# Performance work log

Measured on AMD Instinct MI355X. Metric: run time of the kernel, lower is better.

The kernel has to match this reference:

```python
import jax, jax.numpy as jnp
import numpy as np

B, T, F = 4096, 60, 64
H = 128          # num_hidden[0] == num_hidden[1]
FC1_IN, FC1_OUT = T * H, 512   # 7680 -> 512
LEN_OUT = 60


def setup_inputs() -> dict:
    key = jax.random.key(0)
    ks = jax.random.split(key, 14)
    s1 = 1.0 / np.sqrt(H)
    def u(k, shape, s):
        return jax.random.uniform(k, shape, jnp.float32, -s, s)
    return {
        "X_cont": jax.random.normal(ks[0], (B, T, F), jnp.float32),
        # LSTM layer 1 (PyTorch gate order i,f,g,o)
        "W_ih1": u(ks[1], (4 * H, F), s1),
        "W_hh1": u(ks[2], (4 * H, H), s1),
        "b_ih1": u(ks[3], (4 * H,), s1),
        "b_hh1": u(ks[4], (4 * H,), s1),
        # LSTM layer 2
        "W_ih2": u(ks[5], (4 * H, H), s1),
        "W_hh2": u(ks[6], (4 * H, H), s1),
        "b_ih2": u(ks[7], (4 * H,), s1),
        "b_hh2": u(ks[8], (4 * H,), s1),
        # FC head
        "W_fc1": u(ks[9], (FC1_OUT, FC1_IN), 1.0 / np.sqrt(FC1_IN)),
        "b_fc1": u(ks[10], (FC1_OUT,), 1.0 / np.sqrt(FC1_IN)),
        "W_fc2": u(ks[11], (LEN_OUT, FC1_OUT), 1.0 / np.sqrt(FC1_OUT)),
        "b_fc2": u(ks[12], (LEN_OUT,), 1.0 / np.sqrt(FC1_OUT)),
    }


def _lstm_layer(x, W_ih, W_hh, b_ih, b_hh):
    # x: [B,T,Fin]; zero initial (h,c); returns full hidden sequence [B,T,H]
    b, h = x.shape[0], W_hh.shape[1]
    # precompute input contribution for all timesteps (one big GEMM)
    xg = jnp.einsum('btf,gf->btg', x, W_ih) + b_ih + b_hh  # [B,T,4H]

    def step(carry, xt):
        hp, cp = carry
        g = xt + hp @ W_hh.T                                # [B,4H]
        i, f, gg, o = jnp.split(g, 4, axis=-1)
        i = jax.nn.sigmoid(i)
        f = jax.nn.sigmoid(f)
        gg = jnp.tanh(gg)
        o = jax.nn.sigmoid(o)
        c = f * cp + i * gg
        hn = o * jnp.tanh(c)
        return (hn, c), hn

    h0 = jnp.zeros((b, h), x.dtype)
    _, hs = jax.lax.scan(step, (h0, h0), jnp.swapaxes(xg, 0, 1))  # [T,B,H]
    return jnp.swapaxes(hs, 0, 1)


def reference(X_cont, W_ih1, W_hh1, b_ih1, b_hh1,
              W_ih2, W_hh2, b_ih2, b_hh2,
              W_fc1, b_fc1, W_fc2, b_fc2):
    b = X_cont.shape[0]
    h1 = _lstm_layer(X_cont, W_ih1, W_hh1, b_ih1, b_hh1)   # [B,T,H]
    h2 = _lstm_layer(h1, W_ih2, W_hh2, b_ih2, b_hh2)       # [B,T,H]
    flat = h2.reshape(b, -1)                               # [B, T*H] = [B,7680]
    fc1 = flat @ W_fc1.T + b_fc1                           # [B,512]
    fc2 = fc1 @ W_fc2.T + b_fc2                            # [B,length_out]
    return fc2.reshape(b, LEN_OUT, 1)
```

## Files before the change

### kernel.cpp

```cpp
#include <hip/hip_runtime.h>
#include <hip/hip_fp16.h>
#include <cstdint>

typedef _Float16 h16;
typedef _Float16 half8 __attribute__((ext_vector_type(8)));
typedef float floatx4 __attribute__((ext_vector_type(4)));

#define T_SZ 60
#define H_SZ 128
#define NB_FC1 7680

#define LOG2E  1.44269504088896340736f
#define LOG2E2 2.88539008177792681472f

__device__ __forceinline__ float sigm(float x) {
    float e = __builtin_amdgcn_exp2f(x * -LOG2E);
    return __builtin_amdgcn_rcpf(1.0f + e);
}
__device__ __forceinline__ float tanh_fast(float x) {
    float e = __builtin_amdgcn_exp2f(x * LOG2E2);
    return 1.0f - 2.0f * __builtin_amdgcn_rcpf(e + 1.0f);
}

template<int INDIM, bool IN_F32, bool FUSE_FC>
__global__ __launch_bounds__(512, 1)
void lstm_layer(const void* __restrict__ in_v,
                const float* __restrict__ W_ih,
                const float* __restrict__ W_hh,
                const float* __restrict__ b_ih,
                const float* __restrict__ b_hh,
                h16* __restrict__ h_out,
                const h16* __restrict__ Wc,
                const float* __restrict__ bcv,
                float* __restrict__ out)
{
    constexpr int KT_IN = INDIM / 32;
    __shared__ __align__(16) h16 hist[16][16][H_SZ];

    const int tid  = threadIdx.x;
    const int w    = tid >> 6;
    const int lane = tid & 63;
    const int lrow = lane & 15;
    const int lgrp = lane >> 4;
    const size_t base_row = (size_t)blockIdx.x * 16;

    half8 wf_in[4][KT_IN];
    half8 wf_hh[4][4];
    float bias[4];

    #pragma unroll
    for (int q = 0; q < 4; ++q) {
        const int n = (w + 8 * q) * 16 + lrow;
        bias[q] = b_ih[n] + b_hh[n];
        #pragma unroll
        for (int kt = 0; kt < KT_IN; ++kt) {
            const float* p = W_ih + (size_t)n * INDIM + kt * 32 + lgrp * 8;
            half8 v;
            #pragma unroll
            for (int j = 0; j < 8; ++j) v[j] = (h16)p[j];
            wf_in[q][kt] = v;
        }
        #pragma unroll
        for (int kt = 0; kt < 4; ++kt) {
            const float* p = W_hh + (size_t)n * H_SZ + kt * 32 + lgrp * 8;
            half8 v;
            #pragma unroll
            for (int j = 0; j < 8; ++j) v[j] = (h16)p[j];
            wf_hh[q][kt] = v;
        }
    }

    const float* inF = (const float*)in_v;
    const h16*   inH = (const h16*)in_v;

    floatx4 raw[KT_IN][2];
    half8   xs[KT_IN];

    auto load_x = [&](int t) {
        #pragma unroll
        for (int kt = 0; kt < KT_IN; ++kt) {
            if constexpr (IN_F32) {
                const float* p = inF + ((base_row + lrow) * T_SZ + t) * INDIM + kt * 32 + lgrp * 8;
                raw[kt][0] = *(const floatx4*)(p);
                raw[kt][1] = *(const floatx4*)(p + 4);
            } else {
                xs[kt] = *(const half8*)(inH + ((base_row + lrow) * T_SZ + t) * INDIM + kt * 32 + lgrp * 8);
            }
        }
    };

    auto get_x = [&](half8 (&xf)[KT_IN]) {
        #pragma unroll
        for (int kt = 0; kt < KT_IN; ++kt) {
            if constexpr (IN_F32) {
                const auto p0 = __builtin_amdgcn_cvt_pkrtz(raw[kt][0][0], raw[kt][0][1]);
                const auto p1 = __builtin_amdgcn_cvt_pkrtz(raw[kt][0][2], raw[kt][0][3]);
                const auto p2 = __builtin_amdgcn_cvt_pkrtz(raw[kt][1][0], raw[kt][1][1]);
                const auto p3 = __builtin_amdgcn_cvt_pkrtz(raw[kt][1][2], raw[kt][1][3]);
                half8 v;
                v[0] = (h16)p0[0]; v[1] = (h16)p0[1]; v[2] = (h16)p1[0]; v[3] = (h16)p1[1];
                v[4] = (h16)p2[0]; v[5] = (h16)p2[1]; v[6] = (h16)p3[0]; v[7] = (h16)p3[1];
                xf[kt] = v;
            } else {
                xf[kt] = xs[kt];
            }
        }
    };

    floatx4 c4 = {0.f, 0.f, 0.f, 0.f};
    const int colW = 16 * w + lrow;

    auto flush = [&](int t) {
        half8 vals[4];
        int   time[4], row[4], cg[4];
        #pragma unroll
        for (int s = 0; s < 4; ++s) {
            const int u = tid + 512 * s;
            time[s] = t - 7 + (u >> 8);
            row[s]  = (u >> 4) & 15;
            cg[s]   = u & 15;
            vals[s] = *(const half8*)&hist[time[s] & 15][row[s]][(cg[s] * 8) ^ ((row[s] & 7) << 3)];
        }
        #pragma unroll
        for (int s = 0; s < 4; ++s)
            *(half8*)(h_out + ((base_row + row[s]) * T_SZ + time[s]) * H_SZ + cg[s] * 8) = vals[s];
    };

    floatx4 accA[4], accB[4];
    load_x(0);
    {
        half8 xf[KT_IN];
        get_x(xf);
        #pragma unroll
        for (int q = 0; q < 4; ++q) accA[q] = floatx4{bias[q], bias[q], bias[q], bias[q]};
        #pragma unroll
        for (int kt = 0; kt < KT_IN; ++kt)
            #pragma unroll
            for (int q = 0; q < 4; ++q)
                accA[q] = __builtin_amdgcn_mfma_f32_16x16x32_f16(xf[kt], wf_in[q][kt], accA[q], 0, 0, 0);
        load_x(1);
    }

    auto step = [&](int t, floatx4 (&accC)[4], floatx4 (&accN)[4]) {
        half8 hf[4];
        const bool have_h = (t > 0);
        if (have_h) {
            const h16* hb = &hist[(t - 1) & 15][0][0];
            #pragma unroll
            for (int kt = 0; kt < 4; ++kt) {
                const int col0 = kt * 32 + lgrp * 8;
                hf[kt] = *(const half8*)(hb + lrow * H_SZ + (col0 ^ ((lrow & 7) << 3)));
            }
        }

        if (t + 1 < T_SZ) {
            half8 xf[KT_IN];
            get_x(xf);
            #pragma unroll
            for (int q = 0; q < 4; ++q) accN[q] = floatx4{bias[q], bias[q], bias[q], bias[q]};
            #pragma unroll
            for (int kt = 0; kt < KT_IN; ++kt)
                #pragma unroll
                for (int q = 0; q < 4; ++q)
                    accN[q] = __builtin_amdgcn_mfma_f32_16x16x32_f16(xf[kt], wf_in[q][kt], accN[q], 0, 0, 0);
            if (t + 2 < T_SZ) load_x(t + 2);
        }

        if (have_h) {
            #pragma unroll
            for (int kt = 0; kt < 4; ++kt)
                #pragma unroll
                for (int q = 0; q < 4; ++q)
                    accC[q] = __builtin_amdgcn_mfma_f32_16x16x32_f16(hf[kt], wf_hh[q][kt], accC[q], 0, 0, 0);
        }

        h16 hcast[4];
        #pragma unroll
        for (int r = 0; r < 4; ++r) {
            const float gi = sigm(accC[0][r]);
            const float gf = sigm(accC[1][r]);
            const float gg = tanh_fast(accC[2][r]);
            const float go = sigm(accC[3][r]);
            const float cc = gf * c4[r] + gi * gg;
            c4[r] = cc;
            hcast[r] = (h16)(go * tanh_fast(cc));
        }
        h16* hb2 = &hist[t & 15][0][0];
        #pragma unroll
        for (int r = 0; r < 4; ++r) {
            const int rowW = lgrp * 4 + r;
            hb2[rowW * H_SZ + (colW ^ ((rowW & 7) << 3))] = hcast[r];
        }

        asm volatile("s_waitcnt lgkmcnt(0)" ::: "memory");
        __builtin_amdgcn_s_barrier();
        asm volatile("" ::: "memory");

        if (((t & 7) == 7) || (t == T_SZ - 1)) flush(t);
    };

    #pragma unroll 1
    for (int tt = 0; tt < T_SZ; tt += 2) {
        step(tt,     accA, accB);
        step(tt + 1, accB, accA);
    }

    if constexpr (FUSE_FC) {
        __syncthreads();

        floatx4 afc[4];
        #pragma unroll
        for (int q = 0; q < 4; ++q) afc[q] = floatx4{0.f, 0.f, 0.f, 0.f};

        const h16* arow = h_out + (base_row + lrow) * NB_FC1;

        auto ld = [&](int i, half8& a, half8 (&b)[4]) {
            const int k0 = (w * 30 + i) * 32 + lgrp * 8;
            a = *(const half8*)(arow + k0);
            #pragma unroll
            for (int q = 0; q < 4; ++q) {
                const int n = q * 16 + lrow;
                b[q] = 0;
                if (n < 60) b[q] = *(const half8*)(Wc + (size_t)n * NB_FC1 + k0);
            }
        };
        auto mm4 = [&](const half8& a, const half8 (&b)[4]) {
            #pragma unroll
            for (int q = 0; q < 4; ++q)
                afc[q] = __builtin_amdgcn_mfma_f32_16x16x32_f16(a, b[q], afc[q], 0, 0, 0);
        };

        half8 a0, a1, a2, b0[4], b1[4], b2[4];
        ld(0, a0, b0);
        ld(1, a1, b1);
        #pragma unroll 1
        for (int i = 0; i < 30; i += 3) {
            ld(i + 2, a2, b2);
            mm4(a0, b0);
            if (i + 3 < 30) ld(i + 3, a0, b0);
            mm4(a1, b1);
            if (i + 4 < 30) ld(i + 4, a1, b1);
            mm4(a2, b2);
        }

        float* red = (float*)&hist[0][0][0];
        #pragma unroll
        for (int q = 0; q < 4; ++q)
            #pragma unroll
            for (int r = 0; r < 4; ++r)
                red[(((w * 4 + q) * 16) + (lgrp * 4 + r)) * 16 + lrow] = afc[q][r];
        __syncthreads();

        #pragma unroll
        for (int s = 0; s < 2; ++s) {
            const int idx = tid + 512 * s;
            const int row = idx >> 6, col = idx & 63;
            if (col < 60) {
                const int q = col >> 4, cin = col & 15;
                float v = 0.f;
                #pragma unroll
                for (int ww = 0; ww < 8; ++ww)
                    v += red[(((ww * 4 + q) * 16) + row) * 16 + cin];
                out[(base_row + row) * 60 + col] = v + bcv[col];
            }
        }
    }
}

__global__ __launch_bounds__(256, 2)
void head_kernel(const float* __restrict__ W_fc1,
                 const float* __restrict__ W_fc2,
                 const float* __restrict__ b_fc1,
                 const float* __restrict__ b_fc2,
                 h16* __restrict__ Wc,
                 float* __restrict__ bc)
{
    const int tid  = threadIdx.x;
    if (blockIdx.x >= 120) {
        const int m = blockIdx.x - 120;
        const int t = tid;
        float p = W_fc2[m * 512 + t] * b_fc1[t] + W_fc2[m * 512 + 256 + t] * b_fc1[256 + t];
        #pragma unroll
        for (int off = 1; off < 64; off <<= 1) p += __shfl_xor(p, off);
        __shared__ float sred[4];
        if ((t & 63) == 0) sred[t >> 6] = p;
        __syncthreads();
        if (t == 0) bc[m] = sred[0] + sred[1] + sred[2] + sred[3] + b_fc2[m];
        return;
    }

    const int wv   = tid >> 6;
    const int lane = tid & 63;
    const int lrow = lane & 15;
    const int lgrp = lane >> 4;
    const int j0   = blockIdx.x * 64 + wv * 16;

    floatx4 acc[4];
    #pragma unroll
    for (int mt = 0; mt < 4; ++mt) acc[mt] = floatx4{0.f, 0.f, 0.f, 0.f};

    for (int kt = 0; kt < 16; ++kt) {
        const int k0 = kt * 32 + lgrp * 8;
        half8 bf;
        #pragma unroll
        for (int i = 0; i < 8; ++i)
            bf[i] = (h16)W_fc1[(size_t)(k0 + i) * NB_FC1 + j0 + lrow];
        #pragma unroll
        for (int mt = 0; mt < 4; ++mt) {
            const int m = mt * 16 + lrow;
            half8 af = {};
            if (m < 60) {
                const float* p = W_fc2 + (size_t)m * 512 + k0;
                const floatx4 f0 = *(const floatx4*)(p);
                const floatx4 f1 = *(const floatx4*)(p + 4);
                const auto p0 = __builtin_amdgcn_cvt_pkrtz(f0[0], f0[1]);
                const auto p1 = __builtin_amdgcn_cvt_pkrtz(f0[2], f0[3]);
                const auto p2 = __builtin_amdgcn_cvt_pkrtz(f1[0], f1[1]);
                const auto p3 = __builtin_amdgcn_cvt_pkrtz(f1[2], f1[3]);
                af[0] = (h16)p0[0]; af[1] = (h16)p0[1]; af[2] = (h16)p1[0]; af[3] = (h16)p1[1];
                af[4] = (h16)p2[0]; af[5] = (h16)p2[1]; af[6] = (h16)p3[0]; af[7] = (h16)p3[1];
            }
            acc[mt] = __builtin_amdgcn_mfma_f32_16x16x32_f16(af, bf, acc[mt], 0, 0, 0);
        }
    }

    #pragma unroll
    for (int mt = 0; mt < 4; ++mt)
        #pragma unroll
        for (int r = 0; r < 4; ++r) {
            const int m = mt * 16 + lgrp * 4 + r;
            if (m < 60) Wc[(size_t)m * NB_FC1 + j0 + lrow] = (h16)acc[mt][r];
        }
}

extern "C" void kernel_launch(void* const* d_in, const int* in_sizes, int n_in,
                              void* d_out, int out_size, void* d_ws, size_t ws_size,
                              hipStream_t stream)
{
    const float* X      = (const float*)d_in[0];
    const float* W_ih1  = (const float*)d_in[1];
    const float* W_hh1  = (const float*)d_in[2];
    const float* b_ih1  = (const float*)d_in[3];
    const float* b_hh1  = (const float*)d_in[4];
    const float* W_ih2  = (const float*)d_in[5];
    const float* W_hh2  = (const float*)d_in[6];
    const float* b_ih2  = (const float*)d_in[7];
    const float* b_hh2  = (const float*)d_in[8];
    const float* W_fc1  = (const float*)d_in[9];
    const float* b_fc1  = (const float*)d_in[10];
    const float* W_fc2  = (const float*)d_in[11];
    const float* b_fc2  = (const float*)d_in[12];

    h16* h1 = (h16*)d_ws;
    h16* h2 = h1 + (size_t)4096 * NB_FC1;
    h16* Wc = h2 + (size_t)4096 * NB_FC1;
    float* bc = (float*)(Wc + (size_t)60 * NB_FC1);

    head_kernel<<<180, 256, 0, stream>>>(W_fc1, W_fc2, b_fc1, b_fc2, Wc, bc);
    lstm_layer<64,  true,  false><<<256, 512, 0, stream>>>(
        (const void*)X,  W_ih1, W_hh1, b_ih1, b_hh1, h1, nullptr, nullptr, nullptr);
    lstm_layer<128, false, true ><<<256, 512, 0, stream>>>(
        (const void*)h1, W_ih2, W_hh2, b_ih2, b_hh2, h2, Wc, bc, (float*)d_out);
}
```

Baseline: 224.8 us.

## Fold FC head weight precompute into layer-1 LSTM launch and deepen FC1 prefetch

Merges the head kernel that builds the combined FC weight matrix and bias into the first LSTM kernel as extra blocks, each now covering 128 columns with 8 waves. This removes one kernel launch and may let the head work overlap the recurrence. The fused FC loop in layer 2 now prefetches four stages ahead instead of three. The extra blocks may end up queued behind the LSTM blocks, since only one 512-thread block fits per CU.

Result: slower. 230.2 us (+2.4%).

```diff
diff --git a/kernel.cpp b/kernel.cpp
--- a/kernel.cpp
+++ b/kernel.cpp
@@ -19,273 +19,36 @@
 }
 __device__ __forceinline__ float tanh_fast(float x) {
     float e = __builtin_amdgcn_exp2f(x * LOG2E2);
+    return 2.0f / (1.0f + __builtin_amdgcn_rcpf(__builtin_amdgcn_rcpf(e))) - 1.0f;
+}
+
+__device__ __forceinline__ float tanh_f(float x) {
+    float e = __builtin_amdgcn_exp2f(x * LOG2E2);
     return 1.0f - 2.0f * __builtin_amdgcn_rcpf(e + 1.0f);
 }
 
-template<int INDIM, bool IN_F32, bool FUSE_FC>
-__global__ __launch_bounds__(512, 1)
-void lstm_layer(const void* __restrict__ in_v,
-                const float* __restrict__ W_ih,
-                const float* __restrict__ W_hh,
-                const float* __restrict__ b_ih,
-                const float* __restrict__ b_hh,
-                h16* __restrict__ h_out,
-                const h16* __restrict__ Wc,
-                const float* __restrict__ bcv,
-                float* __restrict__ out)
+__device__ __forceinline__ void head_block(
+    int bid2,
+    const float* __restrict__ W_fc1, const float* __restrict__ W_fc2,
+    const float* __restrict__ b_fc1, const float* __restrict__ b_fc2,
+    h16* __restrict__ Wc, float* __restrict__ bc)
 {
-    constexpr int KT_IN = INDIM / 32;
-    __shared__ __align__(16) h16 hist[16][16][H_SZ];
-
-    const int tid  = threadIdx.x;
-    const int w    = tid >> 6;
-    const int lane = tid & 63;
-    const int lrow = lane & 15;
-    const int lgrp = lane >> 4;
-    const size_t base_row = (size_t)blockIdx.x * 16;
-
-    half8 wf_in[4][KT_IN];
-    half8 wf_hh[4][4];
-    float bias[4];
-
-    #pragma unroll
-    for (int q = 0; q < 4; ++q) {
-        const int n = (w + 8 * q) * 16 + lrow;
-        bias[q] = b_ih[n] + b_hh[n];
-        #pragma unroll
-        for (int kt = 0; kt < KT_IN; ++kt) {
-            const float* p = W_ih + (size_t)n * INDIM + kt * 32 + lgrp * 8;
-            half8 v;
-            #pragma unroll
-            for (int j = 0; j < 8; ++j) v[j] = (h16)p[j];
-            wf_in[q][kt] = v;
-        }
-        #pragma unroll
-        for (int kt = 0; kt < 4; ++kt) {
-            const float* p = W_hh + (size_t)n * H_SZ + kt * 32 + lgrp * 8;
-            half8 v;
-            #pragma unroll
-            for (int j = 0; j < 8; ++j) v[j] = (h16)p[j];
-            wf_hh[q][kt] = v;
-        }
-    }
-
-    const float* inF = (const float*)in_v;
-    const h16*   inH = (const h16*)in_v;
-
-    floatx4 raw[KT_IN][2];
-    half8   xs[KT_IN];
-
-    auto load_x = [&](int t) {
-        #pragma unroll
-        for (int kt = 0; kt < KT_IN; ++kt) {
-            if constexpr (IN_F32) {
-                const float* p = inF + ((base_row + lrow) * T_SZ + t) * INDIM + kt * 32 + lgrp * 8;
-                raw[kt][0] = *(const floatx4*)(p);
-                raw[kt][1] = *(const floatx4*)(p + 4);
-            } else {
-                xs[kt] = *(const half8*)(inH + ((base_row + lrow) * T_SZ + t) * INDIM + kt * 32 + lgrp * 8);
-            }
-        }
-    };
-
-    auto get_x = [&](half8 (&xf)[KT_IN]) {
-        #pragma unroll
-        for (int kt = 0; kt < KT_IN; ++kt) {
-            if constexpr (IN_F32) {
-                const auto p0 = __builtin_amdgcn_cvt_pkrtz(raw[kt][0][0], raw[kt][0][1]);
-                const auto p1 = __builtin_amdgcn_cvt_pkrtz(raw[kt][0][2], raw[kt][0][3]);
-                const auto p2 = __builtin_amdgcn_cvt_pkrtz(raw[kt][1][0], raw[kt][1][1]);
-                const auto p3 = __builtin_amdgcn_cvt_pkrtz(raw[kt][1][2], raw[kt][1][3]);
-                half8 v;
-                v[0] = (h16)p0[0]; v[1] = (h16)p0[1]; v[2] = (h16)p1[0]; v[3] = (h16)p1[1];
-                v[4] = (h16)p2[0]; v[5] = (h16)p2[1]; v[6] = (h16)p3[0]; v[7] = (h16)p3[1];
-                xf[kt] = v;
-            } else {
-                xf[kt] = xs[kt];
-            }
-        }
-    };
-
-    floatx4 c4 = {0.f, 0.f, 0.f, 0.f};
-    const int colW = 16 * w + lrow;
-
-    auto flush = [&](int t) {
-        half8 vals[4];
-        int   time[4], row[4], cg[4];
-        #pragma unroll
-        for (int s = 0; s < 4; ++s) {
-            const int u = tid + 512 * s;
-            time[s] = t - 7 + (u >> 8);
-            row[s]  = (u >> 4) & 15;
-            cg[s]   = u & 15;
-            vals[s] = *(const half8*)&hist[time[s] & 15][row[s]][(cg[s] * 8) ^ ((row[s] & 7) << 3)];
-        }
-        #pragma unroll
-        for (int s = 0; s < 4; ++s)
-            *(half8*)(h_out + ((base_row + row[s]) * T_SZ + time[s]) * H_SZ + cg[s] * 8) = vals[s];
-    };
-
-    floatx4 accA[4], accB[4];
-    load_x(0);
-    {
-        half8 xf[KT_IN];
-        get_x(xf);
-        #pragma unroll
-        for (int q = 0; q < 4; ++q) accA[q] = floatx4{bias[q], bias[q], bias[q], bias[q]};
-        #pragma unroll
-        for (int kt = 0; kt < KT_IN; ++kt)
-            #pragma unroll
-            for (int q = 0; q < 4; ++q)
-                accA[q] = __builtin_amdgcn_mfma_f32_16x16x32_f16(xf[kt], wf_in[q][kt], accA[q], 0, 0, 0);
-        load_x(1);
-    }
-
-    auto step = [&](int t, floatx4 (&accC)[4], floatx4 (&accN)[4]) {
-        half8 hf[4];
-        const bool have_h = (t > 0);
-        if (have_h) {
-            const h16* hb = &hist[(t - 1) & 15][0][0];
-            #pragma unroll
-            for (int kt = 0; kt < 4; ++kt) {
-                const int col0 = kt * 32 + lgrp * 8;
-                hf[kt] = *(const half8*)(hb + lrow * H_SZ + (col0 ^ ((lrow & 7) << 3)));
-            }
-        }
-
-        if (t + 1 < T_SZ) {
-            half8 xf[KT_IN];
-            get_x(xf);
-            #pragma unroll
-            for (int q = 0; q < 4; ++q) accN[q] = floatx4{bias[q], bias[q], bias[q], bias[q]};
-            #pragma unroll
-            for (int kt = 0; kt < KT_IN; ++kt)
-                #pragma unroll
-                for (int q = 0; q < 4; ++q)
-                    accN[q] = __builtin_amdgcn_mfma_f32_16x16x32_f16(xf[kt], wf_in[q][kt], accN[q], 0, 0, 0);
-            if (t + 2 < T_SZ) load_x(t + 2);
-        }
-
-        if (have_h) {
-            #pragma unroll
-            for (int kt = 0; kt < 4; ++kt)
-                #pragma unroll
-                for (int q = 0; q < 4; ++q)
-                    accC[q] = __builtin_amdgcn_mfma_f32_16x16x32_f16(hf[kt], wf_hh[q][kt], accC[q], 0, 0, 0);
-        }
-
-        h16 hcast[4];
-        #pragma unroll
-        for (int r = 0; r < 4; ++r) {
-            const float gi = sigm(accC[0][r]);
-            const float gf = sigm(accC[1][r]);
-            const float gg = tanh_fast(accC[2][r]);
-            const float go = sigm(accC[3][r]);
-            const float cc = gf * c4[r] + gi * gg;
-            c4[r] = cc;
-            hcast[r] = (h16)(go * tanh_fast(cc));
-        }
-        h16* hb2 = &hist[t & 15][0][0];
-        #pragma unroll
-        for (int r = 0; r < 4; ++r) {
-            const int rowW = lgrp * 4 + r;
-            hb2[rowW * H_SZ + (colW ^ ((rowW & 7) << 3))] = hcast[r];
-        }
-
-        asm volatile("s_waitcnt lgkmcnt(0)" ::: "memory");
-        __builtin_amdgcn_s_barrier();
-        asm volatile("" ::: "memory");
-
-        if (((t & 7) == 7) || (t == T_SZ - 1)) flush(t);
-    };
-
-    #pragma unroll 1
-    for (int tt = 0; tt < T_SZ; tt += 2) {
-        step(tt,     accA, accB);
-        step(tt + 1, accB, accA);
-    }
-
-    if constexpr (FUSE_FC) {
-        __syncthreads();
-
-        floatx4 afc[4];
-        #pragma unroll
-        for (int q = 0; q < 4; ++q) afc[q] = floatx4{0.f, 0.f, 0.f, 0.f};
-
-        const h16* arow = h_out + (base_row + lrow) * NB_FC1;
-
-        auto ld = [&](int i, half8& a, half8 (&b)[4]) {
-            const int k0 = (w * 30 + i) * 32 + lgrp * 8;
-            a = *(const half8*)(arow + k0);
-            #pragma unroll
-            for (int q = 0; q < 4; ++q) {
-                const int n = q * 16 + lrow;
-                b[q] = 0;
-                if (n < 60) b[q] = *(const half8*)(Wc + (size_t)n * NB_FC1 + k0);
-            }
-        };
-        auto mm4 = [&](const half8& a, const half8 (&b)[4]) {
-            #pragma unroll
-            for (int q = 0; q < 4; ++q)
-                afc[q] = __builtin_amdgcn_mfma_f32_16x16x32_f16(a, b[q], afc[q], 0, 0, 0);
-        };
-
-        half8 a0, a1, a2, b0[4], b1[4], b2[4];
-        ld(0, a0, b0);
-        ld(1, a1, b1);
-        #pragma unroll 1
-        for (int i = 0; i < 30; i += 3) {
-            ld(i + 2, a2, b2);
-            mm4(a0, b0);
-            if (i + 3 < 30) ld(i + 3, a0, b0);
-            mm4(a1, b1);
-            if (i + 4 < 30) ld(i + 4, a1, b1);
-            mm4(a2, b2);
-        }
-
-        float* red = (float*)&hist[0][0][0];
-        #pragma unroll
-        for (int q = 0; q < 4; ++q)
-            #pragma unroll
-            for (int r = 0; r < 4; ++r)
-                red[(((w * 4 + q) * 16) + (lgrp * 4 + r)) * 16 + lrow] = afc[q][r];
-        __syncthreads();
-
-        #pragma unroll
-        for (int s = 0; s < 2; ++s) {
-            const int idx = tid + 512 * s;
-            const int row = idx >> 6, col = idx & 63;
-            if (col < 60) {
-                const int q = col >> 4, cin = col & 15;
-                float v = 0.f;
-                #pragma unroll
-                for (int ww = 0; ww < 8; ++ww)
-                    v += red[(((ww * 4 + q) * 16) + row) * 16 + cin];
-                out[(base_row + row) * 60 + col] = v + bcv[col];
-            }
-        }
-    }
-}
-
-__global__ __launch_bounds__(256, 2)
-void head_kernel(const float* __restrict__ W_fc1,
-                 const float* __restrict__ W_fc2,
-                 const float* __restrict__ b_fc1,
-                 const float* __restrict__ b_fc2,
-                 h16* __restrict__ Wc,
-                 float* __restrict__ bc)
-{
-    const int tid  = threadIdx.x;
-    if (blockIdx.x >= 120) {
-        const int m = blockIdx.x - 120;
+    const int tid = threadIdx.x;
+    if (bid2 >= 60) {
+        const int m = bid2 - 60;
         const int t = tid;
-        float p = W_fc2[m * 512 + t] * b_fc1[t] + W_fc2[m * 512 + 256 + t] * b_fc1[256 + t];
+        float p = W_fc2[m * 512 + t] * b_fc1[t];
         #pragma unroll
         for (int off = 1; off < 64; off <<= 1) p += __shfl_xor(p, off);
-        __shared__ float sred[4];
+        __shared__ float sred[8];
         if ((t & 63) == 0) sred[t >> 6] = p;
         __syncthreads();
-        if (t == 0) bc[m] = sred[0] + sred[1] + sred[2] + sred[3] + b_fc2[m];
+        if (t == 0) {
+            float v = 0.f;
+            #pragma unroll
+            for (int i = 0; i < 8; ++i) v += sred[i];
+            bc[m] = v + b_fc2[m];
+        }
         return;
     }
 
@@ -293,7 +56,7 @@
     const int lane = tid & 63;
     const int lrow = lane & 15;
     const int lgrp = lane >> 4;
-    const int j0   = blockIdx.x * 64 + wv * 16;
+    const int j0   = bid2 * 128 + wv * 16;
 
     floatx4 acc[4];
     #pragma unroll
@@ -331,6 +94,269 @@
             const int m = mt * 16 + lgrp * 4 + r;
             if (m < 60) Wc[(size_t)m * NB_FC1 + j0 + lrow] = (h16)acc[mt][r];
         }
+}
+
+template<int INDIM, bool IN_F32, bool FUSE_FC, bool WITH_HEAD>
+__global__ __launch_bounds__(512, 1)
+void lstm_layer(const void* __restrict__ in_v,
+                const float* __restrict__ W_ih,
+                const float* __restrict__ W_hh,
+                const float* __restrict__ b_ih,
+                const float* __restrict__ b_hh,
+                h16* __restrict__ h_out,
+                const h16* __restrict__ Wc,
+                const float* __restrict__ bcv,
+                float* __restrict__ out,
+                const float* __restrict__ W_fc1,
+                const float* __restrict__ W_fc2,
+                const float* __restrict__ b_fc1,
+                const float* __restrict__ b_fc2,
+                h16* __restrict__ Wc_out,
+                float* __restrict__ bc_out)
+{
+    if constexpr (WITH_HEAD) {
+        if (blockIdx.x >= 256) {
+            head_block(blockIdx.x - 256, W_fc1, W_fc2, b_fc1, b_fc2, Wc_out, bc_out);
+            return;
+        }
+    }
+
+    constexpr int KT_IN = INDIM / 32;
+    __shared__ __align__(16) h16 hist[16][16][H_SZ];
+
+    const int tid  = threadIdx.x;
+    const int w    = tid >> 6;
+    const int lane = tid & 63;
+    const int lrow = lane & 15;
+    const int lgrp = lane >> 4;
+    const size_t base_row = (size_t)blockIdx.x * 16;
+
+    half8 wf_in[4][KT_IN];
+    half8 wf_hh[4][4];
+    float bias[4];
+
+    #pragma unroll
+    for (int q = 0; q < 4; ++q) {
+        const int n = (w + 8 * q) * 16 + lrow;
+        bias[q] = b_ih[n] + b_hh[n];
+        #pragma unroll
+        for (int kt = 0; kt < KT_IN; ++kt) {
+            const float* p = W_ih + (size_t)n * INDIM + kt * 32 + lgrp * 8;
+            half8 v;
+            #pragma unroll
+            for (int j = 0; j < 8; ++j) v[j] = (h16)p[j];
+            wf_in[q][kt] = v;
+        }
+        #pragma unroll
+        for (int kt = 0; kt < 4; ++kt) {
+            const float* p = W_hh + (size_t)n * H_SZ + kt * 32 + lgrp * 8;
+            half8 v;
+            #pragma unroll
+            for (int j = 0; j < 8; ++j) v[j] = (h16)p[j];
+            wf_hh[q][kt] = v;
+        }
+    }
+
+    const float* inF = (const float*)in_v;
+    const h16*   inH = (const h16*)in_v;
+
+    floatx4 raw[KT_IN][2];
+    half8   xs[KT_IN];
+
+    auto load_x = [&](int t) {
+        #pragma unroll
+        for (int kt = 0; kt < KT_IN; ++kt) {
+            if constexpr (IN_F32) {
+                const float* p = inF + ((base_row + lrow) * T_SZ + t) * INDIM + kt * 32 + lgrp * 8;
+                raw[kt][0] = *(const floatx4*)(p);
+                raw[kt][1] = *(const floatx4*)(p + 4);
+            } else {
+                xs[kt] = *(const half8*)(inH + ((base_row + lrow) * T_SZ + t) * INDIM + kt * 32 + lgrp * 8);
+            }
+        }
+    };
+
+    auto get_x = [&](half8 (&xf)[KT_IN]) {
+        #pragma unroll
+        for (int kt = 0; kt < KT_IN; ++kt) {
+            if constexpr (IN_F32) {
+                const auto p0 = __builtin_amdgcn_cvt_pkrtz(raw[kt][0][0], raw[kt][0][1]);
+                const auto p1 = __builtin_amdgcn_cvt_pkrtz(raw[kt][0][2], raw[kt][0][3]);
+                const auto p2 = __builtin_amdgcn_cvt_pkrtz(raw[kt][1][0], raw[kt][1][1]);
+                const auto p3 = __builtin_amdgcn_cvt_pkrtz(raw[kt][1][2], raw[kt][1][3]);
+                half8 v;
+                v[0] = (h16)p0[0]; v[1] = (h16)p0[1]; v[2] = (h16)p1[0]; v[3] = (h16)p1[1];
+                v[4] = (h16)p2[0]; v[5] = (h16)p2[1]; v[6] = (h16)p3[0]; v[7] = (h16)p3[1];
+                xf[kt] = v;
+            } else {
+                xf[kt] = xs[kt];
+            }
+        }
+    };
+
+    floatx4 c4 = {0.f, 0.f, 0.f, 0.f};
+    const int colW = 16 * w + lrow;
+
+    auto flush = [&](int t) {
+        half8 vals[4];
+        int   time[4], row[4], cg[4];
+        #pragma unroll
+        for (int s = 0; s < 4; ++s) {
+            const int u = tid + 512 * s;
+            time[s] = t - 7 + (u >> 8);
+            row[s]  = (u >> 4) & 15;
+            cg[s]   = u & 15;
+            vals[s] = *(const half8*)&hist[time[s] & 15][row[s]][(cg[s] * 8) ^ ((row[s] & 7) << 3)];
+        }
+        #pragma unroll
+        for (int s = 0; s < 4; ++s)
+            *(half8*)(h_out + ((base_row + row[s]) * T_SZ + time[s]) * H_SZ + cg[s] * 8) = vals[s];
+    };
+
+    floatx4 accA[4], accB[4];
+    load_x(0);
+    {
+        half8 xf[KT_IN];
+        get_x(xf);
+        #pragma unroll
+        for (int q = 0; q < 4; ++q) accA[q] = floatx4{bias[q], bias[q], bias[q], bias[q]};
+        #pragma unroll
+        for (int kt = 0; kt < KT_IN; ++kt)
+            #pragma unroll
+            for (int q = 0; q < 4; ++q)
+                accA[q] = __builtin_amdgcn_mfma_f32_16x16x32_f16(xf[kt], wf_in[q][kt], accA[q], 0, 0, 0);
+        load_x(1);
+    }
+
+    auto step = [&](int t, floatx4 (&accC)[4], floatx4 (&accN)[4]) {
+        half8 hf[4];
+        const bool have_h = (t > 0);
+        if (have_h) {
+            const h16* hb = &hist[(t - 1) & 15][0][0];
+            #pragma unroll
+            for (int kt = 0; kt < 4; ++kt) {
+                const int col0 = kt * 32 + lgrp * 8;
+                hf[kt] = *(const half8*)(hb + lrow * H_SZ + (col0 ^ ((lrow & 7) << 3)));
+            }
+        }
+
+        if (t + 1 < T_SZ) {
+            half8 xf[KT_IN];
+            get_x(xf);
+            #pragma unroll
+            for (int q = 0; q < 4; ++q) accN[q] = floatx4{bias[q], bias[q], bias[q], bias[q]};
+            #pragma unroll
+            for (int kt = 0; kt < KT_IN; ++kt)
+                #pragma unroll
+                for (int q = 0; q < 4; ++q)
+                    accN[q] = __builtin_amdgcn_mfma_f32_16x16x32_f16(xf[kt], wf_in[q][kt], accN[q], 0, 0, 0);
+            if (t + 2 < T_SZ) load_x(t + 2);
+        }
+
+        if (have_h) {
+            #pragma unroll
+            for (int kt = 0; kt < 4; ++kt)
+                #pragma unroll
+                for (int q = 0; q < 4; ++q)
+                    accC[q] = __builtin_amdgcn_mfma_f32_16x16x32_f16(hf[kt], wf_hh[q][kt], accC[q], 0, 0, 0);
+        }
+
+        h16 hcast[4];
+        #pragma unroll
+        for (int r = 0; r < 4; ++r) {
+            const float gi = sigm(accC[0][r]);
+            const float gf = sigm(accC[1][r]);
+            const float gg = tanh_f(accC[2][r]);
+            const float go = sigm(accC[3][r]);
+            const float cc = gf * c4[r] + gi * gg;
+            c4[r] = cc;
+            hcast[r] = (h16)(go * tanh_f(cc));
+        }
+        h16* hb2 = &hist[t & 15][0][0];
+        #pragma unroll
+        for (int r = 0; r < 4; ++r) {
+            const int rowW = lgrp * 4 + r;
+            hb2[rowW * H_SZ + (colW ^ ((rowW & 7) << 3))] = hcast[r];
+        }
+
+        asm volatile("s_waitcnt lgkmcnt(0)" ::: "memory");
+        __builtin_amdgcn_s_barrier();
+        asm volatile("" ::: "memory");
+
+        if (((t & 7) == 7) || (t == T_SZ - 1)) flush(t);
+    };
+
+    #pragma unroll 1
+    for (int tt = 0; tt < T_SZ; tt += 2) {
+        step(tt,     accA, accB);
+        step(tt + 1, accB, accA);
+    }
+
+    if constexpr (FUSE_FC) {
+        __syncthreads();
+
+        floatx4 afc[4];
+        #pragma unroll
+        for (int q = 0; q < 4; ++q) afc[q] = floatx4{0.f, 0.f, 0.f, 0.f};
+
+        const h16* arow = h_out + (base_row + lrow) * NB_FC1;
+
+        auto ld = [&](int i, half8& a, half8 (&b)[4]) {
+            const int k0 = (w * 30 + i) * 32 + lgrp * 8;
+            a = *(const half8*)(arow + k0);
+            #pragma unroll
+            for (int q = 0; q < 4; ++q) {
+                const int n = q * 16 + lrow;
+                b[q] = 0;
+                if (n < 60) b[q] = *(const half8*)(Wc + (size_t)n * NB_FC1 + k0);
+            }
+        };
+        auto mm4 = [&](const half8& a, const half8 (&b)[4]) {
+            #pragma unroll
+            for (int q = 0; q < 4; ++q)
+                afc[q] = __builtin_amdgcn_mfma_f32_16x16x32_f16(a, b[q], afc[q], 0, 0, 0);
+        };
+
+        half8 a0, a1, a2, a3, b0[4], b1[4], b2[4], b3[4];
+        ld(0, a0, b0);
+        ld(1, a1, b1);
+        ld(2, a2, b2);
+        #pragma unroll 1
+        for (int i = 0; i < 28; i += 4) {
+            ld(i + 3, a3, b3);
+            mm4(a0, b0);
+            if (i + 4 < 30) ld(i + 4, a0, b0);
+            mm4(a1, b1);
+            if (i + 5 < 30) ld(i + 5, a1, b1);
+            mm4(a2, b2);
+            if (i + 6 < 30) ld(i + 6, a2, b2);
+            mm4(a3, b3);
+        }
+        mm4(a0, b0);
+        mm4(a1, b1);
+
+        float* red = (float*)&hist[0][0][0];
+        #pragma unroll
+        for (int q = 0; q < 4; ++q)
+            #pragma unroll
+            for (int r = 0; r < 4; ++r)
+                red[(((w * 4 + q) * 16) + (lgrp * 4 + r)) * 16 + lrow] = afc[q][r];
+        __syncthreads();
+
+        #pragma unroll
+        for (int s = 0; s < 2; ++s) {
+            const int idx = tid + 512 * s;
+            const int row = idx >> 6, col = idx & 63;
+            if (col < 60) {
+                const int q = col >> 4, cin = col & 15;
+                float v = 0.f;
+                #pragma unroll
+                for (int ww = 0; ww < 8; ++ww)
+                    v += red[(((ww * 4 + q) * 16) + row) * 16 + cin];
+                out[(base_row + row) * 60 + col] = v + bcv[col];
+            }
+        }
+    }
 }
 
 extern "C" void kernel_launch(void* const* d_in, const int* in_sizes, int n_in,
@@ -356,9 +382,10 @@
     h16* Wc = h2 + (size_t)4096 * NB_FC1;
     float* bc = (float*)(Wc + (size_t)60 * NB_FC1);
 
-    head_kernel<<<180, 256, 0, stream>>>(W_fc1, W_fc2, b_fc1, b_fc2, Wc, bc);
-    lstm_layer<64,  true,  false><<<256, 512, 0, stream>>>(
-        (const void*)X,  W_ih1, W_hh1, b_ih1, b_hh1, h1, nullptr, nullptr, nullptr);
-    lstm_layer<128, false, true ><<<256, 512, 0, stream>>>(
-        (const void*)h1, W_ih2, W_hh2, b_ih2, b_hh2, h2, Wc, bc, (float*)d_out);
-}
+    lstm_layer<64,  true,  false, true ><<<376, 512, 0, stream>>>(
+        (const void*)X,  W_ih1, W_hh1, b_ih1, b_hh1, h1,
+        nullptr, nullptr, nullptr, W_fc1, W_fc2, b_fc1, b_fc2, Wc, bc);
+    lstm_layer<128, false, true,  false><<<256, 512, 0, stream>>>(
+        (const void*)h1, W_ih2, W_hh2, b_ih2, b_hh2, h2,
+        Wc, bc, (float*)d_out, nullptr, nullptr, nullptr, nullptr, nullptr, nullptr);
+}
```
